# Performance work log

Hardware: AMD Instinct MI355X
Metric: run time of the kernel (lower is better)

The kernel has to match this reference:

```python
import jax, jax.numpy as jnp
import numpy as np

C = 128  # channel dim, forced equal to W by the reshape logic

def conv1x1(x, w, b):
    # 1x1 conv == per-pixel channel GEMM
    return jnp.einsum('bhwc,cd->bhwd', x, w) + b

def setup_inputs() -> dict:
    key = jax.random.key(0)
    ks = jax.random.split(key, 6)
    B, H, W = 8, 256, 128
    s = 1.0 / np.sqrt(C)
    return {
        'x': jax.random.normal(ks[0], (B, H, W, C), jnp.float32),
        'w_theta': jax.random.normal(ks[1], (C, C), jnp.float32) * s,
        'b_theta': jnp.zeros((C,), jnp.float32),
        'w_phi': jax.random.normal(ks[2], (C, C), jnp.float32) * s,
        'b_phi': jnp.zeros((C,), jnp.float32),
        'w_g': jax.random.normal(ks[3], (C, C), jnp.float32) * s,
        'b_g': jnp.zeros((C,), jnp.float32),
        'w_sc': jax.random.normal(ks[4], (C, C), jnp.float32) * s,
        'b_sc': jnp.zeros((C,), jnp.float32),
        'w_out': jax.random.normal(ks[5], (3 * C, C), jnp.float32) * (1.0 / np.sqrt(3 * C)),
        'b_out': jnp.zeros((C,), jnp.float32),
    }

def reference(x, w_theta, b_theta, w_phi, b_phi, w_g, b_g, w_sc, b_sc, w_out, b_out):
    B, H, W, Cc = x.shape  # W == Cc == 128 by construction
    f_theta = conv1x1(x, w_theta, b_theta)
    f_phi = conv1x1(x, w_phi, b_phi)
    f_g = conv1x1(x, w_g, b_g)
    # flatten (B,H) into batch of row-strips, each [W, C]
    ft = f_theta.reshape(B * H, W, Cc)
    fp = f_phi.reshape(B * H, W, Cc)
    fg = f_g.reshape(B * H, W, Cc)
    # horizontal: sigmoid(phi @ theta^T) -> [B*H, W, W] -> [B,H,W,C] (W==C)
    h_att = jax.nn.sigmoid(jnp.einsum('nwc,nvc->nwv', fp, ft)).reshape(B, H, W, Cc)
    horizontal_result = h_att * x
    # vertical: sigmoid(g^T @ phi) -> [B*H, C, C] -> [B,H,W,C]
    v_att = jax.nn.sigmoid(jnp.einsum('nwc,nwd->ncd', fg, fp)).reshape(B, H, W, Cc)
    vertical_result = v_att * x
    short_cut = conv1x1(x, w_sc, b_sc)
    cab = jnp.concatenate([horizontal_result, short_cut, vertical_result], axis=-1)
    return conv1x1(cab, w_out, b_out)
```

## Files before the change

### kernel.cpp

```cpp
#include <hip/hip_runtime.h>


typedef __bf16 bf16x8 __attribute__((ext_vector_type(8)));
typedef __bf16 bf16x4 __attribute__((ext_vector_type(4)));
typedef float f32x16 __attribute__((ext_vector_type(16)));

__device__ __forceinline__ int swz(int row, int cb) {
    return (row << 8) + (cb ^ ((row & 15) << 4));
}
__device__ __forceinline__ float sigm(float t) {
    return 1.0f / (1.0f + __expf(-t));
}

__global__ void prep_combine(const float* __restrict__ w_sc,
                             const float* __restrict__ b_sc,
                             const float* __restrict__ w_out,
                             const float* __restrict__ b_out,
                             float* __restrict__ wsc2,
                             float* __restrict__ bout2) {
    int k = blockIdx.x;
    int n = threadIdx.x;
    float acc = 0.f;
    for (int c = 0; c < 128; ++c)
        acc += w_sc[k * 128 + c] * w_out[(128 + c) * 128 + n];
    wsc2[k * 128 + n] = acc;
    if (k == 0) {
        float b = b_out[n];
        for (int c = 0; c < 128; ++c)
            b += b_sc[c] * w_out[(128 + c) * 128 + n];
        bout2[n] = b;
    }
}

__global__ void prep_pack(const float* __restrict__ wth,
                          const float* __restrict__ wph,
                          const float* __restrict__ wg,
                          const float* __restrict__ wout,
                          const float* __restrict__ wsc2,
                          __bf16* __restrict__ packs) {
    int m = blockIdx.x;
    const float* src;
    int rowoff = 0;
    if (m == 0) src = wth;
    else if (m == 1) src = wph;
    else if (m == 2) src = wg;
    else if (m == 3) { src = wout; rowoff = 0; }
    else if (m == 4) { src = wout; rowoff = 256; }
    else src = wsc2;
    __bf16* dst = packs + m * 16384;
    for (int i = threadIdx.x; i < 16384; i += blockDim.x) {
        int j = i & 7;
        int lane = (i >> 3) & 63;
        int kk = (i >> 9) & 7;
        int nt = i >> 12;
        int k = kk * 16 + ((lane >> 5) << 3) + j;
        int n = nt * 32 + (lane & 31);
        dst[i] = (__bf16)(src[(rowoff + k) * 128 + n]);
    }
}

#define FPB 32768
#define FGT 98304

__global__ __launch_bounds__(1024, 1)
void cab_main(const float* __restrict__ x,
              const float* __restrict__ b_theta,
              const float* __restrict__ b_phi,
              const float* __restrict__ b_g,
              const __bf16* __restrict__ packs,
              const float* __restrict__ bout2,
              float* __restrict__ out,
              int nstrips, int spb) {
    __shared__ __align__(16) char lds[131072];

    const int tid = threadIdx.x;
    const int l   = tid & 63;
    const int wv  = tid >> 6;
    const int ct  = wv & 3;
    const int rt  = wv >> 2;
    const int ln  = l & 31;
    const int lh  = l >> 5;
    const int colg = ct * 32 + ln;
    const int m0   = rt * 32;

    const __bf16* pTH = packs;
    const __bf16* pPH = packs + 16384;
    const __bf16* pG  = packs + 2 * 16384;
    const __bf16* pO0 = packs + 3 * 16384;
    const __bf16* pO2 = packs + 4 * 16384;
    const __bf16* pS2 = packs + 5 * 16384;

    const float biasTH = b_theta[colg];
    const float biasPH = b_phi[colg];
    const float biasG  = b_g[colg];
    const float biasO  = bout2[colg];

    const int s0 = blockIdx.x * spb;
    if (s0 >= nstrips) return;
    const float4* x4 = (const float4*)x;

    const int srow = tid >> 5;
    const int scb  = (tid & 31) * 8;

    float4 pf[2];

    {
        long base = (long)s0 * 4096;
#pragma unroll
        for (int c = 0; c < 2; ++c) {
#pragma unroll
            for (int q = 0; q < 2; ++q) pf[q] = x4[base + (c * 2 + q) * 1024 + tid];
#pragma unroll
            for (int q = 0; q < 2; ++q) {
                int row = (c * 2 + q) * 32 + srow;
                bf16x4 v;
                v[0] = (__bf16)pf[q].x; v[1] = (__bf16)pf[q].y;
                v[2] = (__bf16)pf[q].z; v[3] = (__bf16)pf[q].w;
                *(bf16x4*)(lds + swz(row, scb)) = v;
            }
        }
    }
    __syncthreads();

    for (int it = 0; it < spb; ++it) {
        const int s = s0 + it;
        const int XBo  = (it & 1) ? 65536 : 0;
        const int FPTo = 65536 - XBo;
        f32x16 acc;

#pragma unroll
        for (int i = 0; i < 16; ++i) acc[i] = 0.f;
#pragma unroll 2
        for (int kk = 0; kk < 8; ++kk) {
            bf16x8 b = *(const bf16x8*)(pPH + (((ct * 8 + kk) * 64 + l) << 3));
            bf16x8 a = *(const bf16x8*)(lds + XBo + swz(m0 + ln, kk * 32 + lh * 16));
            acc = __builtin_amdgcn_mfma_f32_32x32x16_bf16(a, b, acc, 0, 0, 0);
        }
#pragma unroll
        for (int r = 0; r < 16; ++r) {
            int row = m0 + (r & 3) + ((r >> 2) << 3) + (lh << 2);
            *(__bf16*)(lds + FPB + swz(row, colg * 2)) = (__bf16)(acc[r] + biasPH);
        }
#pragma unroll
        for (int q = 0; q < 4; ++q) {
            int w0 = m0 + (q << 3) + (lh << 2);
            bf16x4 v;
#pragma unroll
            for (int e = 0; e < 4; ++e) v[e] = (__bf16)(acc[q * 4 + e] + biasPH);
            *(bf16x4*)(lds + FPTo + swz(colg, w0 * 2)) = v;
        }

#pragma unroll
        for (int i = 0; i < 16; ++i) acc[i] = 0.f;
#pragma unroll 2
        for (int kk = 0; kk < 8; ++kk) {
            bf16x8 b = *(const bf16x8*)(pG + (((ct * 8 + kk) * 64 + l) << 3));
            bf16x8 a = *(const bf16x8*)(lds + XBo + swz(m0 + ln, kk * 32 + lh * 16));
            acc = __builtin_amdgcn_mfma_f32_32x32x16_bf16(a, b, acc, 0, 0, 0);
        }
#pragma unroll
        for (int q = 0; q < 4; ++q) {
            int w0 = m0 + (q << 3) + (lh << 2);
            bf16x4 v;
#pragma unroll
            for (int e = 0; e < 4; ++e) v[e] = (__bf16)(acc[q * 4 + e] + biasG);
            *(bf16x4*)(lds + FGT + swz(colg, w0 * 2)) = v;
        }
        __syncthreads();

        if (it + 1 < spb) {
            long base = (long)(s + 1) * 4096;
#pragma unroll
            for (int q = 0; q < 2; ++q) pf[q] = x4[base + q * 1024 + tid];
        }

#pragma unroll
        for (int i = 0; i < 16; ++i) acc[i] = 0.f;
#pragma unroll 2
        for (int kk = 0; kk < 8; ++kk) {
            bf16x8 b = *(const bf16x8*)(lds + FGT + swz(colg, kk * 32 + lh * 16));
            bf16x8 a = *(const bf16x8*)(lds + FPTo + swz(m0 + ln, kk * 32 + lh * 16));
            acc = __builtin_amdgcn_mfma_f32_32x32x16_bf16(a, b, acc, 0, 0, 0);
        }
        __syncthreads();

#pragma unroll
        for (int q = 0; q < 4; ++q) {
            int j0 = m0 + (q << 3) + (lh << 2);
            bf16x4 xv = *(const bf16x4*)(lds + XBo + swz(colg, j0 * 2));
            bf16x4 v;
#pragma unroll
            for (int e = 0; e < 4; ++e)
                v[e] = (__bf16)(sigm(acc[q * 4 + e]) * (float)xv[e]);
            *(bf16x4*)(lds + FGT + swz(colg, j0 * 2)) = v;
        }

#pragma unroll
        for (int i = 0; i < 16; ++i) acc[i] = 0.f;
#pragma unroll 2
        for (int kk = 0; kk < 8; ++kk) {
            bf16x8 b = *(const bf16x8*)(pTH + (((ct * 8 + kk) * 64 + l) << 3));
            bf16x8 a = *(const bf16x8*)(lds + XBo + swz(m0 + ln, kk * 32 + lh * 16));
            acc = __builtin_amdgcn_mfma_f32_32x32x16_bf16(a, b, acc, 0, 0, 0);
        }
#pragma unroll
        for (int r = 0; r < 16; ++r) {
            int row = m0 + (r & 3) + ((r >> 2) << 3) + (lh << 2);
            *(__bf16*)(lds + FPTo + swz(row, colg * 2)) = (__bf16)(acc[r] + biasTH);
        }
        __syncthreads();

#pragma unroll
        for (int i = 0; i < 16; ++i) acc[i] = 0.f;
#pragma unroll 2
        for (int kk = 0; kk < 8; ++kk) {
            bf16x8 b = *(const bf16x8*)(lds + FPB + swz(colg, kk * 32 + lh * 16));
            bf16x8 a = *(const bf16x8*)(lds + FPTo + swz(m0 + ln, kk * 32 + lh * 16));
            acc = __builtin_amdgcn_mfma_f32_32x32x16_bf16(a, b, acc, 0, 0, 0);
        }
        __syncthreads();

        if (it + 1 < spb) {
#pragma unroll
            for (int q = 0; q < 2; ++q) {
                int row = q * 32 + srow;
                bf16x4 v;
                v[0] = (__bf16)pf[q].x; v[1] = (__bf16)pf[q].y;
                v[2] = (__bf16)pf[q].z; v[3] = (__bf16)pf[q].w;
                *(bf16x4*)(lds + FPTo + swz(row, scb)) = v;
            }
            long base = (long)(s + 1) * 4096;
#pragma unroll
            for (int q = 0; q < 2; ++q) pf[q] = x4[base + (2 + q) * 1024 + tid];
        }

#pragma unroll
        for (int q = 0; q < 4; ++q) {
            int v0 = m0 + (q << 3) + (lh << 2);
            bf16x4 xv = *(const bf16x4*)(lds + XBo + swz(colg, v0 * 2));
            bf16x4 v;
#pragma unroll
            for (int e = 0; e < 4; ++e)
                v[e] = (__bf16)(sigm(acc[q * 4 + e]) * (float)xv[e]);
            *(bf16x4*)(lds + FPB + swz(colg, v0 * 2)) = v;
        }
        __syncthreads();

#pragma unroll
        for (int i = 0; i < 16; ++i) acc[i] = 0.f;
#pragma unroll 2
        for (int kk = 0; kk < 8; ++kk) {
            bf16x8 b = *(const bf16x8*)(pO0 + (((ct * 8 + kk) * 64 + l) << 3));
            bf16x8 a = *(const bf16x8*)(lds + FPB + swz(m0 + ln, kk * 32 + lh * 16));
            acc = __builtin_amdgcn_mfma_f32_32x32x16_bf16(a, b, acc, 0, 0, 0);
        }
#pragma unroll 2
        for (int kk = 0; kk < 8; ++kk) {
            bf16x8 b = *(const bf16x8*)(pO2 + (((ct * 8 + kk) * 64 + l) << 3));
            bf16x8 a = *(const bf16x8*)(lds + FGT + swz(m0 + ln, kk * 32 + lh * 16));
            acc = __builtin_amdgcn_mfma_f32_32x32x16_bf16(a, b, acc, 0, 0, 0);
        }
#pragma unroll 2
        for (int kk = 0; kk < 8; ++kk) {
            bf16x8 b = *(const bf16x8*)(pS2 + (((ct * 8 + kk) * 64 + l) << 3));
            bf16x8 a = *(const bf16x8*)(lds + XBo + swz(m0 + ln, kk * 32 + lh * 16));
            acc = __builtin_amdgcn_mfma_f32_32x32x16_bf16(a, b, acc, 0, 0, 0);
        }
        {
            long obase = (long)s * 16384;
#pragma unroll
            for (int r = 0; r < 16; ++r) {
                int row = m0 + (r & 3) + ((r >> 2) << 3) + (lh << 2);
                out[obase + row * 128 + colg] = acc[r] + biasO;
            }
        }

        if (it + 1 < spb) {
#pragma unroll
            for (int q = 0; q < 2; ++q) {
                int row = 64 + q * 32 + srow;
                bf16x4 v;
                v[0] = (__bf16)pf[q].x; v[1] = (__bf16)pf[q].y;
                v[2] = (__bf16)pf[q].z; v[3] = (__bf16)pf[q].w;
                *(bf16x4*)(lds + FPTo + swz(row, scb)) = v;
            }
        }
        __syncthreads();
    }
}

extern "C" void kernel_launch(void* const* d_in, const int* in_sizes, int n_in,
                              void* d_out, int out_size, void* d_ws, size_t ws_size,
                              hipStream_t stream) {
    const float* x       = (const float*)d_in[0];
    const float* w_theta = (const float*)d_in[1];
    const float* b_theta = (const float*)d_in[2];
    const float* w_phi   = (const float*)d_in[3];
    const float* b_phi   = (const float*)d_in[4];
    const float* w_g     = (const float*)d_in[5];
    const float* b_g     = (const float*)d_in[6];
    const float* w_sc    = (const float*)d_in[7];
    const float* b_sc    = (const float*)d_in[8];
    const float* w_out   = (const float*)d_in[9];
    const float* b_out   = (const float*)d_in[10];
    float* out = (float*)d_out;

    float* wsc2 = (float*)d_ws;
    __bf16* packs = (__bf16*)((char*)d_ws + 65536);
    float* bout2 = (float*)((char*)d_ws + 65536 + 6 * 16384 * 2);

    int NS = in_sizes[0] / 16384;
    int spb = NS / 256;
    if (spb < 1) spb = 1;
    int grid = (NS + spb - 1) / spb;

    prep_combine<<<128, 128, 0, stream>>>(w_sc, b_sc, w_out, b_out, wsc2, bout2);
    prep_pack<<<6, 256, 0, stream>>>(w_theta, w_phi, w_g, w_out, wsc2, packs);
    cab_main<<<grid, 1024, 0, stream>>>(x, b_theta, b_phi, b_g, packs, bout2, out, NS, spb);
}
```

Baseline: 174.8 us.

## Halve block to 512 threads with 32x64 per-wave tiles and register-cached x fragments

Reworks the main kernel from 16 waves each owning one 32x32 output tile to 8 waves each owning two adjacent 32x32 tiles, so every A fragment feeds two MFMAs. The x-strip A fragments are loaded into registers once per strip and reused across the phi, g, theta and shortcut GEMMs. __syncthreads is replaced by a raw lgkmcnt wait plus s_barrier, and sched_barrier hints are added. The goal is to cut LDS traffic and barrier cost, at the price of higher register pressure. The block still uses 128 KB of LDS, so the requested two blocks per CU may not actually fit.

Measured after the change: 391.6 us. 2.24x slower.

```diff
diff --git a/kernel.cpp b/kernel.cpp
--- a/kernel.cpp
+++ b/kernel.cpp
@@ -10,6 +10,11 @@
 }
 __device__ __forceinline__ float sigm(float t) {
     return 1.0f / (1.0f + __expf(-t));
+}
+__device__ __forceinline__ void bar() {
+    asm volatile("s_waitcnt lgkmcnt(0)" ::: "memory");
+    __builtin_amdgcn_s_barrier();
+    asm volatile("" ::: "memory");
 }
 
 __global__ void prep_combine(const float* __restrict__ w_sc,
@@ -62,7 +67,7 @@
 #define FPB 32768
 #define FGT 98304
 
-__global__ __launch_bounds__(1024, 1)
+__global__ __launch_bounds__(512, 2)
 void cab_main(const float* __restrict__ x,
               const float* __restrict__ b_theta,
               const float* __restrict__ b_phi,
@@ -76,12 +81,15 @@
     const int tid = threadIdx.x;
     const int l   = tid & 63;
     const int wv  = tid >> 6;
-    const int ct  = wv & 3;
-    const int rt  = wv >> 2;
+    const int rt  = wv >> 1;
+    const int cp  = wv & 1;
     const int ln  = l & 31;
     const int lh  = l >> 5;
-    const int colg = ct * 32 + ln;
-    const int m0   = rt * 32;
+    const int m0    = rt * 32;
+    const int colg0 = cp * 64 + ln;
+    const int colg1 = colg0 + 32;
+    const int c0    = cp * 2;
+    const int c1    = c0 + 1;
 
     const __bf16* pTH = packs;
     const __bf16* pPH = packs + 16384;
@@ -90,10 +98,10 @@
     const __bf16* pO2 = packs + 4 * 16384;
     const __bf16* pS2 = packs + 5 * 16384;
 
-    const float biasTH = b_theta[colg];
-    const float biasPH = b_phi[colg];
-    const float biasG  = b_g[colg];
-    const float biasO  = bout2[colg];
+    const float biasTH0 = b_theta[colg0], biasTH1 = b_theta[colg1];
+    const float biasPH0 = b_phi[colg0],   biasPH1 = b_phi[colg1];
+    const float biasG0  = b_g[colg0],     biasG1  = b_g[colg1];
+    const float biasO0  = bout2[colg0],   biasO1  = bout2[colg1];
 
     const int s0 = blockIdx.x * spb;
     if (s0 >= nstrips) return;
@@ -102,17 +110,17 @@
     const int srow = tid >> 5;
     const int scb  = (tid & 31) * 8;
 
-    float4 pf[2];
+    float4 pf[4];
 
     {
         long base = (long)s0 * 4096;
 #pragma unroll
         for (int c = 0; c < 2; ++c) {
 #pragma unroll
-            for (int q = 0; q < 2; ++q) pf[q] = x4[base + (c * 2 + q) * 1024 + tid];
-#pragma unroll
-            for (int q = 0; q < 2; ++q) {
-                int row = (c * 2 + q) * 32 + srow;
+            for (int q = 0; q < 4; ++q) pf[q] = x4[base + (c * 4 + q) * 512 + tid];
+#pragma unroll
+            for (int q = 0; q < 4; ++q) {
+                int row = c * 64 + q * 16 + srow;
                 bf16x4 v;
                 v[0] = (__bf16)pf[q].x; v[1] = (__bf16)pf[q].y;
                 v[2] = (__bf16)pf[q].z; v[3] = (__bf16)pf[q].w;
@@ -120,110 +128,148 @@
             }
         }
     }
-    __syncthreads();
+    bar();
 
     for (int it = 0; it < spb; ++it) {
         const int s = s0 + it;
         const int XBo  = (it & 1) ? 65536 : 0;
         const int FPTo = 65536 - XBo;
-        f32x16 acc;
-
-#pragma unroll
-        for (int i = 0; i < 16; ++i) acc[i] = 0.f;
+        f32x16 accA, accB;
+
+        bf16x8 xf[8];
+#pragma unroll
+        for (int kk = 0; kk < 8; ++kk)
+            xf[kk] = *(const bf16x8*)(lds + XBo + swz(m0 + ln, kk * 32 + lh * 16));
+
+#pragma unroll
+        for (int i = 0; i < 16; ++i) { accA[i] = 0.f; accB[i] = 0.f; }
+#pragma unroll
+        for (int j = 0; j < 8; ++j) {
+            bf16x8 b0 = *(const bf16x8*)(pPH + (((c0 * 8 + j) * 64 + l) << 3));
+            bf16x8 b1 = *(const bf16x8*)(pPH + (((c1 * 8 + j) * 64 + l) << 3));
+            accA = __builtin_amdgcn_mfma_f32_32x32x16_bf16(xf[j], b0, accA, 0, 0, 0);
+            accB = __builtin_amdgcn_mfma_f32_32x32x16_bf16(xf[j], b1, accB, 0, 0, 0);
+            if (j & 1) __builtin_amdgcn_sched_barrier(0);
+        }
+#pragma unroll
+        for (int t = 0; t < 2; ++t) {
+            const f32x16& acc = t ? accB : accA;
+            int cg = colg0 + t * 32;
+            float bias = t ? biasPH1 : biasPH0;
+#pragma unroll
+            for (int r = 0; r < 16; ++r) {
+                int row = m0 + (r & 3) + ((r >> 2) << 3) + (lh << 2);
+                *(__bf16*)(lds + FPB + swz(row, cg * 2)) = (__bf16)(acc[r] + bias);
+            }
+#pragma unroll
+            for (int q = 0; q < 4; ++q) {
+                int w0 = m0 + (q << 3) + (lh << 2);
+                bf16x4 v;
+#pragma unroll
+                for (int e = 0; e < 4; ++e) v[e] = (__bf16)(acc[q * 4 + e] + bias);
+                *(bf16x4*)(lds + FPTo + swz(cg, w0 * 2)) = v;
+            }
+        }
+
+#pragma unroll
+        for (int i = 0; i < 16; ++i) { accA[i] = 0.f; accB[i] = 0.f; }
+#pragma unroll
+        for (int j = 0; j < 8; ++j) {
+            bf16x8 b0 = *(const bf16x8*)(pG + (((c0 * 8 + j) * 64 + l) << 3));
+            bf16x8 b1 = *(const bf16x8*)(pG + (((c1 * 8 + j) * 64 + l) << 3));
+            accA = __builtin_amdgcn_mfma_f32_32x32x16_bf16(xf[j], b0, accA, 0, 0, 0);
+            accB = __builtin_amdgcn_mfma_f32_32x32x16_bf16(xf[j], b1, accB, 0, 0, 0);
+            if (j & 1) __builtin_amdgcn_sched_barrier(0);
+        }
+#pragma unroll
+        for (int t = 0; t < 2; ++t) {
+            const f32x16& acc = t ? accB : accA;
+            int cg = colg0 + t * 32;
+            float bias = t ? biasG1 : biasG0;
+#pragma unroll
+            for (int q = 0; q < 4; ++q) {
+                int w0 = m0 + (q << 3) + (lh << 2);
+                bf16x4 v;
+#pragma unroll
+                for (int e = 0; e < 4; ++e) v[e] = (__bf16)(acc[q * 4 + e] + bias);
+                *(bf16x4*)(lds + FGT + swz(cg, w0 * 2)) = v;
+            }
+        }
+        bar();
+
+        if (it + 1 < spb) {
+            long base = (long)(s + 1) * 4096;
+#pragma unroll
+            for (int q = 0; q < 4; ++q) pf[q] = x4[base + q * 512 + tid];
+        }
+
+#pragma unroll
+        for (int i = 0; i < 16; ++i) { accA[i] = 0.f; accB[i] = 0.f; }
 #pragma unroll 2
         for (int kk = 0; kk < 8; ++kk) {
-            bf16x8 b = *(const bf16x8*)(pPH + (((ct * 8 + kk) * 64 + l) << 3));
-            bf16x8 a = *(const bf16x8*)(lds + XBo + swz(m0 + ln, kk * 32 + lh * 16));
-            acc = __builtin_amdgcn_mfma_f32_32x32x16_bf16(a, b, acc, 0, 0, 0);
-        }
-#pragma unroll
-        for (int r = 0; r < 16; ++r) {
-            int row = m0 + (r & 3) + ((r >> 2) << 3) + (lh << 2);
-            *(__bf16*)(lds + FPB + swz(row, colg * 2)) = (__bf16)(acc[r] + biasPH);
-        }
-#pragma unroll
-        for (int q = 0; q < 4; ++q) {
-            int w0 = m0 + (q << 3) + (lh << 2);
-            bf16x4 v;
-#pragma unroll
-            for (int e = 0; e < 4; ++e) v[e] = (__bf16)(acc[q * 4 + e] + biasPH);
-            *(bf16x4*)(lds + FPTo + swz(colg, w0 * 2)) = v;
-        }
-
-#pragma unroll
-        for (int i = 0; i < 16; ++i) acc[i] = 0.f;
+            bf16x8 a  = *(const bf16x8*)(lds + FPTo + swz(m0 + ln, kk * 32 + lh * 16));
+            bf16x8 b0 = *(const bf16x8*)(lds + FGT + swz(colg0, kk * 32 + lh * 16));
+            bf16x8 b1 = *(const bf16x8*)(lds + FGT + swz(colg1, kk * 32 + lh * 16));
+            accA = __builtin_amdgcn_mfma_f32_32x32x16_bf16(a, b0, accA, 0, 0, 0);
+            accB = __builtin_amdgcn_mfma_f32_32x32x16_bf16(a, b1, accB, 0, 0, 0);
+        }
+        bar();
+
+#pragma unroll
+        for (int t = 0; t < 2; ++t) {
+            const f32x16& acc = t ? accB : accA;
+            int cg = colg0 + t * 32;
+#pragma unroll
+            for (int q = 0; q < 4; ++q) {
+                int j0 = m0 + (q << 3) + (lh << 2);
+                bf16x4 xv = *(const bf16x4*)(lds + XBo + swz(cg, j0 * 2));
+                bf16x4 v;
+#pragma unroll
+                for (int e = 0; e < 4; ++e)
+                    v[e] = (__bf16)(sigm(acc[q * 4 + e]) * (float)xv[e]);
+                *(bf16x4*)(lds + FGT + swz(cg, j0 * 2)) = v;
+            }
+        }
+
+#pragma unroll
+        for (int i = 0; i < 16; ++i) { accA[i] = 0.f; accB[i] = 0.f; }
+#pragma unroll
+        for (int j = 0; j < 8; ++j) {
+            bf16x8 b0 = *(const bf16x8*)(pTH + (((c0 * 8 + j) * 64 + l) << 3));
+            bf16x8 b1 = *(const bf16x8*)(pTH + (((c1 * 8 + j) * 64 + l) << 3));
+            accA = __builtin_amdgcn_mfma_f32_32x32x16_bf16(xf[j], b0, accA, 0, 0, 0);
+            accB = __builtin_amdgcn_mfma_f32_32x32x16_bf16(xf[j], b1, accB, 0, 0, 0);
+            if (j & 1) __builtin_amdgcn_sched_barrier(0);
+        }
+#pragma unroll
+        for (int t = 0; t < 2; ++t) {
+            const f32x16& acc = t ? accB : accA;
+            int cg = colg0 + t * 32;
+            float bias = t ? biasTH1 : biasTH0;
+#pragma unroll
+            for (int r = 0; r < 16; ++r) {
+                int row = m0 + (r & 3) + ((r >> 2) << 3) + (lh << 2);
+                *(__bf16*)(lds + FPTo + swz(row, cg * 2)) = (__bf16)(acc[r] + bias);
+            }
+        }
+        bar();
+
+#pragma unroll
+        for (int i = 0; i < 16; ++i) { accA[i] = 0.f; accB[i] = 0.f; }
 #pragma unroll 2
         for (int kk = 0; kk < 8; ++kk) {
-            bf16x8 b = *(const bf16x8*)(pG + (((ct * 8 + kk) * 64 + l) << 3));
-            bf16x8 a = *(const bf16x8*)(lds + XBo + swz(m0 + ln, kk * 32 + lh * 16));
-            acc = __builtin_amdgcn_mfma_f32_32x32x16_bf16(a, b, acc, 0, 0, 0);
-        }
-#pragma unroll
-        for (int q = 0; q < 4; ++q) {
-            int w0 = m0 + (q << 3) + (lh << 2);
-            bf16x4 v;
-#pragma unroll
-            for (int e = 0; e < 4; ++e) v[e] = (__bf16)(acc[q * 4 + e] + biasG);
-            *(bf16x4*)(lds + FGT + swz(colg, w0 * 2)) = v;
-        }
-        __syncthreads();
+            bf16x8 a  = *(const bf16x8*)(lds + FPTo + swz(m0 + ln, kk * 32 + lh * 16));
+            bf16x8 b0 = *(const bf16x8*)(lds + FPB + swz(colg0, kk * 32 + lh * 16));
+            bf16x8 b1 = *(const bf16x8*)(lds + FPB + swz(colg1, kk * 32 + lh * 16));
+            accA = __builtin_amdgcn_mfma_f32_32x32x16_bf16(a, b0, accA, 0, 0, 0);
+            accB = __builtin_amdgcn_mfma_f32_32x32x16_bf16(a, b1, accB, 0, 0, 0);
+        }
+        bar();
 
         if (it + 1 < spb) {
-            long base = (long)(s + 1) * 4096;
-#pragma unroll
-            for (int q = 0; q < 2; ++q) pf[q] = x4[base + q * 1024 + tid];
-        }
-
-#pragma unroll
-        for (int i = 0; i < 16; ++i) acc[i] = 0.f;
-#pragma unroll 2
-        for (int kk = 0; kk < 8; ++kk) {
-            bf16x8 b = *(const bf16x8*)(lds + FGT + swz(colg, kk * 32 + lh * 16));
-            bf16x8 a = *(const bf16x8*)(lds + FPTo + swz(m0 + ln, kk * 32 + lh * 16));
-            acc = __builtin_amdgcn_mfma_f32_32x32x16_bf16(a, b, acc, 0, 0, 0);
-        }
-        __syncthreads();
-
-#pragma unroll
-        for (int q = 0; q < 4; ++q) {
-            int j0 = m0 + (q << 3) + (lh << 2);
-            bf16x4 xv = *(const bf16x4*)(lds + XBo + swz(colg, j0 * 2));
-            bf16x4 v;
-#pragma unroll
-            for (int e = 0; e < 4; ++e)
-                v[e] = (__bf16)(sigm(acc[q * 4 + e]) * (float)xv[e]);
-            *(bf16x4*)(lds + FGT + swz(colg, j0 * 2)) = v;
-        }
-
-#pragma unroll
-        for (int i = 0; i < 16; ++i) acc[i] = 0.f;
-#pragma unroll 2
-        for (int kk = 0; kk < 8; ++kk) {
-            bf16x8 b = *(const bf16x8*)(pTH + (((ct * 8 + kk) * 64 + l) << 3));
-            bf16x8 a = *(const bf16x8*)(lds + XBo + swz(m0 + ln, kk * 32 + lh * 16));
-            acc = __builtin_amdgcn_mfma_f32_32x32x16_bf16(a, b, acc, 0, 0, 0);
-        }
-#pragma unroll
-        for (int r = 0; r < 16; ++r) {
-            int row = m0 + (r & 3) + ((r >> 2) << 3) + (lh << 2);
-            *(__bf16*)(lds + FPTo + swz(row, colg * 2)) = (__bf16)(acc[r] + biasTH);
-        }
-        __syncthreads();
-
-#pragma unroll
-        for (int i = 0; i < 16; ++i) acc[i] = 0.f;
-#pragma unroll 2
-        for (int kk = 0; kk < 8; ++kk) {
-            bf16x8 b = *(const bf16x8*)(lds + FPB + swz(colg, kk * 32 + lh * 16));
-            bf16x8 a = *(const bf16x8*)(lds + FPTo + swz(m0 + ln, kk * 32 + lh * 16));
-            acc = __builtin_amdgcn_mfma_f32_32x32x16_bf16(a, b, acc, 0, 0, 0);
-        }
-        __syncthreads();
-
-        if (it + 1 < spb) {
-#pragma unroll
-            for (int q = 0; q < 2; ++q) {
-                int row = q * 32 + srow;
+#pragma unroll
+            for (int q = 0; q < 4; ++q) {
+                int row = q * 16 + srow;
                 bf16x4 v;
                 v[0] = (__bf16)pf[q].x; v[1] = (__bf16)pf[q].y;
                 v[2] = (__bf16)pf[q].z; v[3] = (__bf16)pf[q].w;
@@ -231,61 +277,78 @@
             }
             long base = (long)(s + 1) * 4096;
 #pragma unroll
-            for (int q = 0; q < 2; ++q) pf[q] = x4[base + (2 + q) * 1024 + tid];
-        }
-
-#pragma unroll
-        for (int q = 0; q < 4; ++q) {
-            int v0 = m0 + (q << 3) + (lh << 2);
-            bf16x4 xv = *(const bf16x4*)(lds + XBo + swz(colg, v0 * 2));
-            bf16x4 v;
-#pragma unroll
-            for (int e = 0; e < 4; ++e)
-                v[e] = (__bf16)(sigm(acc[q * 4 + e]) * (float)xv[e]);
-            *(bf16x4*)(lds + FPB + swz(colg, v0 * 2)) = v;
-        }
-        __syncthreads();
-
-#pragma unroll
-        for (int i = 0; i < 16; ++i) acc[i] = 0.f;
+            for (int q = 0; q < 4; ++q) pf[q] = x4[base + (4 + q) * 512 + tid];
+        }
+
+#pragma unroll
+        for (int t = 0; t < 2; ++t) {
+            const f32x16& acc = t ? accB : accA;
+            int cg = colg0 + t * 32;
+#pragma unroll
+            for (int q = 0; q < 4; ++q) {
+                int v0 = m0 + (q << 3) + (lh << 2);
+                bf16x4 xv = *(const bf16x4*)(lds + XBo + swz(cg, v0 * 2));
+                bf16x4 v;
+#pragma unroll
+                for (int e = 0; e < 4; ++e)
+                    v[e] = (__bf16)(sigm(acc[q * 4 + e]) * (float)xv[e]);
+                *(bf16x4*)(lds + FPB + swz(cg, v0 * 2)) = v;
+            }
+        }
+        bar();
+
+#pragma unroll
+        for (int i = 0; i < 16; ++i) { accA[i] = 0.f; accB[i] = 0.f; }
 #pragma unroll 2
         for (int kk = 0; kk < 8; ++kk) {
-            bf16x8 b = *(const bf16x8*)(pO0 + (((ct * 8 + kk) * 64 + l) << 3));
-            bf16x8 a = *(const bf16x8*)(lds + FPB + swz(m0 + ln, kk * 32 + lh * 16));
-            acc = __builtin_amdgcn_mfma_f32_32x32x16_bf16(a, b, acc, 0, 0, 0);
+            bf16x8 a  = *(const bf16x8*)(lds + FPB + swz(m0 + ln, kk * 32 + lh * 16));
+            bf16x8 b0 = *(const bf16x8*)(pO0 + (((c0 * 8 + kk) * 64 + l) << 3));
+            bf16x8 b1 = *(const bf16x8*)(pO0 + (((c1 * 8 + kk) * 64 + l) << 3));
+            accA = __builtin_amdgcn_mfma_f32_32x32x16_bf16(a, b0, accA, 0, 0, 0);
+            accB = __builtin_amdgcn_mfma_f32_32x32x16_bf16(a, b1, accB, 0, 0, 0);
         }
 #pragma unroll 2
         for (int kk = 0; kk < 8; ++kk) {
-            bf16x8 b = *(const bf16x8*)(pO2 + (((ct * 8 + kk) * 64 + l) << 3));
-            bf16x8 a = *(const bf16x8*)(lds + FGT + swz(m0 + ln, kk * 32 + lh * 16));
-            acc = __builtin_amdgcn_mfma_f32_32x32x16_bf16(a, b, acc, 0, 0, 0);
-        }
-#pragma unroll 2
-        for (int kk = 0; kk < 8; ++kk) {
-            bf16x8 b = *(const bf16x8*)(pS2 + (((ct * 8 + kk) * 64 + l) << 3));
-            bf16x8 a = *(const bf16x8*)(lds + XBo + swz(m0 + ln, kk * 32 + lh * 16));
-            acc = __builtin_amdgcn_mfma_f32_32x32x16_bf16(a, b, acc, 0, 0, 0);
+            bf16x8 a  = *(const bf16x8*)(lds + FGT + swz(m0 + ln, kk * 32 + lh * 16));
+            bf16x8 b0 = *(const bf16x8*)(pO2 + (((c0 * 8 + kk) * 64 + l) << 3));
+            bf16x8 b1 = *(const bf16x8*)(pO2 + (((c1 * 8 + kk) * 64 + l) << 3));
+            accA = __builtin_amdgcn_mfma_f32_32x32x16_bf16(a, b0, accA, 0, 0, 0);
+            accB = __builtin_amdgcn_mfma_f32_32x32x16_bf16(a, b1, accB, 0, 0, 0);
+        }
+#pragma unroll
+        for (int j = 0; j < 8; ++j) {
+            bf16x8 b0 = *(const bf16x8*)(pS2 + (((c0 * 8 + j) * 64 + l) << 3));
+            bf16x8 b1 = *(const bf16x8*)(pS2 + (((c1 * 8 + j) * 64 + l) << 3));
+            accA = __builtin_amdgcn_mfma_f32_32x32x16_bf16(xf[j], b0, accA, 0, 0, 0);
+            accB = __builtin_amdgcn_mfma_f32_32x32x16_bf16(xf[j], b1, accB, 0, 0, 0);
+            if (j & 1) __builtin_amdgcn_sched_barrier(0);
         }
         {
             long obase = (long)s * 16384;
 #pragma unroll
-            for (int r = 0; r < 16; ++r) {
-                int row = m0 + (r & 3) + ((r >> 2) << 3) + (lh << 2);
-                out[obase + row * 128 + colg] = acc[r] + biasO;
+            for (int t = 0; t < 2; ++t) {
+                const f32x16& acc = t ? accB : accA;
+                int cg = colg0 + t * 32;
+                float bias = t ? biasO1 : biasO0;
+#pragma unroll
+                for (int r = 0; r < 16; ++r) {
+                    int row = m0 + (r & 3) + ((r >> 2) << 3) + (lh << 2);
+                    out[obase + row * 128 + cg] = acc[r] + bias;
+                }
             }
         }
 
         if (it + 1 < spb) {
 #pragma unroll
-            for (int q = 0; q < 2; ++q) {
-                int row = 64 + q * 32 + srow;
+            for (int q = 0; q < 4; ++q) {
+                int row = 64 + q * 16 + srow;
                 bf16x4 v;
                 v[0] = (__bf16)pf[q].x; v[1] = (__bf16)pf[q].y;
                 v[2] = (__bf16)pf[q].z; v[3] = (__bf16)pf[q].w;
                 *(bf16x4*)(lds + FPTo + swz(row, scb)) = v;
             }
         }
-        __syncthreads();
+        bar();
     }
 }
 
@@ -316,5 +379,5 @@
 
     prep_combine<<<128, 128, 0, stream>>>(w_sc, b_sc, w_out, b_out, wsc2, bout2);
     prep_pack<<<6, 256, 0, stream>>>(w_theta, w_phi, w_g, w_out, wsc2, packs);
-    cab_main<<<grid, 1024, 0, stream>>>(x, b_theta, b_phi, b_g, packs, bout2, out, NS, spb);
-}
+    cab_main<<<grid, 512, 0, stream>>>(x, b_theta, b_phi, b_g, packs, bout2, out, NS, spb);
+}
```
